# Optimization experiments

Measured on AMD Instinct MI355X. Metric: run time of the kernel, lower is better.

Reference implementation:

```python
import jax, jax.numpy as jnp
import numpy as np

OFFSET_BINS = np.array([0.0, 0.00794435329, 0.0158887021, 0.0238330509, 0.0317773996,
                        0.0397217484, 0.0476660972, 0.0556104459, 0.0635547947,
                        0.0714991435, 0.08], dtype=np.float32)
BIN_WEIGHTS = jnp.array([0.16652107, 0.21488856, 0.37031708, 0.55618503, 0.75124664,
                         0.93943357, 1.07824539, 1.19423112, 1.55731375, 2.34173634],
                        dtype=jnp.float32)
RADIUS = 0.005
FAR = 1.0e5
EPS = 1e-7


def setup_inputs():
    key = jax.random.key(0)
    ks = jax.random.split(key, 10)
    B, N, M, C = 4, 2048, 4096, 5
    return {
        'pred_grasps': jax.random.normal(ks[0], (B, N, 4, 4), jnp.float32) * 0.1,
        'pred_scores': jax.random.uniform(ks[1], (B, N, 1), jnp.float32, 1e-4, 1.0 - 1e-4),
        'pred_points': jax.random.uniform(ks[2], (B, N, 3), jnp.float32) * 0.1,
        'grasp_width_head': jax.random.normal(ks[3], (B, 10, N), jnp.float32),
        'pos_contact_points': jax.random.uniform(ks[4], (B, M, 3), jnp.float32) * 0.1,
        'pos_contact_width': jax.random.uniform(ks[5], (B, M), jnp.float32) * 0.08,
        'pos_contact_rot': jax.random.normal(ks[6], (B, M, 3, 3), jnp.float32),
        'pos_contact_trans': jax.random.uniform(ks[7], (B, M, 3), jnp.float32) * 0.1,
        'gripper_control_points': jax.random.normal(ks[8], (1, C, 3), jnp.float32) * 0.05,
        'gripper_control_points_sym': jax.random.normal(ks[9], (1, C, 3), jnp.float32) * 0.05,
        'epoch': 0,
    }


def _gather(a, idx):
    # a: (B, M, ...), idx: (B, N) -> (B, N, ...)
    return jax.vmap(lambda x, j: x[j])(a, idx)


def _pairwise_sq(a, b):
    # a: (B,N,3), b: (B,M,3) -> (B,N,M) squared distances via norm expansion
    an = jnp.sum(a * a, -1)
    bn = jnp.sum(b * b, -1)
    cross = jnp.einsum('bnd,bmd->bnm', a, b)
    return jnp.maximum(an[:, :, None] + bn[:, None, :] - 2.0 * cross, 0.0)


def _pair_min_cp(P, G):
    # P,G: (B,N,C,3) control point sets -> (B,N) min_j sum_{c,d}(P_i - G_j)^2
    pn = jnp.sum(P * P, axis=(2, 3))
    gn = jnp.sum(G * G, axis=(2, 3))
    cross = jnp.einsum('bicd,bjcd->bij', P, G)  # (B,N,N)
    sq = pn[:, :, None] + gn[:, None, :] - 2.0 * cross
    return jnp.min(sq, axis=2)


def _forward(pred_grasps, pred_scores, pred_points, grasp_width_head,
             pos_contact_points, pos_contact_width, pos_contact_rot,
             pos_contact_trans, gripper_control_points, gripper_control_points_sym):
    B, N, _ = pred_points.shape
    # ---- labels: nearest GT contact per predicted point (nsample=1) ----
    d2 = _pairwise_sq(pred_points, pos_contact_points)          # (B,N,M)
    idx = jnp.argmin(d2, axis=2)                                 # (B,N)
    min_d2 = jnp.take_along_axis(d2, idx[:, :, None], axis=2)[..., 0]
    width_label = _gather(pos_contact_width, idx)[..., None]     # (B,N,1)
    success = (min_d2 < RADIUS ** 2).astype(jnp.float32)[..., None]  # (B,N,1)
    rot_label = _gather(pos_contact_rot, idx)                    # (B,N,3,3)
    trans_label = _gather(pos_contact_trans, idx)                # (B,N,3)

    pos_in_view = jnp.clip(jnp.sum(success, axis=1), 1.0, None)  # (B,1)

    # ---- binary score loss with balanced pos/neg sampling ----
    p = jnp.clip(pred_scores, EPS, 1.0 - EPS)
    bce = -(success * jnp.log(p) + (1.0 - success) * jnp.log(1.0 - p))[..., 0]  # (B,N)
    pos = success[..., 0]
    neg = 1.0 - pos
    n_pos = jnp.sum(pos, axis=1)                                 # (B,)
    r = jax.random.uniform(jax.random.key(42), (B, N))
    pri = jnp.where(neg > 0.5, r, jnp.inf)
    rank = jnp.argsort(jnp.argsort(pri, axis=1), axis=1)         # random ranks over negatives
    k = jnp.where(n_pos > 0, n_pos, 2.0)
    sel_neg = ((rank < k[:, None]) & (neg > 0.5)).astype(jnp.float32)
    sel = pos + sel_neg
    bin_ce_loss = jnp.mean(jnp.sum(bce * sel, axis=1) / jnp.maximum(jnp.sum(sel, axis=1), 1.0))

    # ---- width loss: multihot bins + weighted BCE-with-logits ----
    lo = jnp.asarray(OFFSET_BINS[:-1])
    hi = jnp.asarray(OFFSET_BINS[1:])
    multihot = ((width_label >= lo) & (width_label < hi)).astype(jnp.float32)  # (B,N,10)
    x = jnp.transpose(grasp_width_head, (0, 2, 1))               # (B,N,10)
    bcew = jnp.maximum(x, 0.0) - x * multihot + jnp.log1p(jnp.exp(-jnp.abs(x)))
    wl = jnp.mean(BIN_WEIGHTS[None, None, :] * bcew, axis=2)     # (B,N)
    width_loss = jnp.mean(jnp.sum(wl * pos, axis=1, keepdims=True) / pos_in_view)

    # ---- ADD-S loss ----
    mask = success > 0.5                                          # (B,N,1)
    rot_l = jnp.where(mask[..., None], rot_label, FAR)
    trans_l = jnp.where(mask, trans_label, FAR)
    cp = gripper_control_points[0]                                # (C,3)
    cps = gripper_control_points_sym[0]
    pred_rot = pred_grasps[:, :, :3, :3]
    pred_trans = pred_grasps[:, :, :3, 3]
    P = jnp.einsum('bnij,cj->bnci', pred_rot, cp) + pred_trans[:, :, None, :]
    G = jnp.einsum('bnij,cj->bnci', rot_l, cp) + trans_l[:, :, None, :]
    Gs = jnp.einsum('bnij,cj->bnci', rot_l, cps) + trans_l[:, :, None, :]
    m = jnp.minimum(_pair_min_cp(P, G), _pair_min_cp(P, Gs))     # (B,N)
    min_adds = pos * jnp.sqrt(jnp.maximum(m, 0.0) + 1e-12)
    adds = jnp.sum(pred_scores[..., 0] * min_adds, axis=1) / pos_in_view[:, 0]
    adds_loss = jnp.mean(adds)

    total_loss = bin_ce_loss + width_loss + 3.0 * adds_loss
    return total_loss, bin_ce_loss, width_loss, adds_loss


def reference(pred_grasps, pred_scores, pred_points, grasp_width_head,
              pos_contact_points, pos_contact_width, pos_contact_rot,
              pos_contact_trans, gripper_control_points, gripper_control_points_sym, epoch):
    return _forward(pred_grasps, pred_scores, pred_points, grasp_width_head,
                    pos_contact_points, pos_contact_width, pos_contact_rot,
                    pos_contact_trans, gripper_control_points, gripper_control_points_sym)
```

## Files before the change

kernel.cpp:

```cpp
#include <hip/hip_runtime.h>
#include <math.h>

#define B_ 4
#define N_ 2048
#define M_ 4096

__constant__ float c_LO[10] = {0.0f, 0.00794435329f, 0.0158887021f, 0.0238330509f,
                               0.0317773996f, 0.0397217484f, 0.0476660972f,
                               0.0556104459f, 0.0635547947f, 0.0714991435f};
__constant__ float c_HI[10] = {0.00794435329f, 0.0158887021f, 0.0238330509f,
                               0.0317773996f, 0.0397217484f, 0.0476660972f,
                               0.0556104459f, 0.0635547947f, 0.0714991435f, 0.08f};
__constant__ float c_BW[10] = {0.16652107f, 0.21488856f, 0.37031708f, 0.55618503f,
                               0.75124664f, 0.93943357f, 1.07824539f, 1.19423112f,
                               1.55731375f, 2.34173634f};

#define R2_ 2.5e-05f
#define FAR_ 100000.0f
#define EPS_ 1e-07f

__device__ inline unsigned rotl32(unsigned x, int d) { return (x << d) | (x >> (32 - d)); }

__device__ inline void threefry2x32_42(unsigned x0, unsigned x1, unsigned& o0, unsigned& o1) {
    const unsigned k0 = 0u, k1 = 42u;
    const unsigned k2 = k0 ^ k1 ^ 0x1BD11BDAu;
    const unsigned ks[3] = {k0, k1, k2};
    const int rot[2][4] = {{13, 15, 26, 6}, {17, 29, 16, 24}};
    unsigned v0 = x0 + k0;
    unsigned v1 = x1 + k1;
#pragma unroll
    for (int i = 0; i < 5; ++i) {
        const int* r = rot[i & 1];
#pragma unroll
        for (int j = 0; j < 4; ++j) {
            v0 += v1;
            v1 = rotl32(v1, r[j]);
            v1 ^= v0;
        }
        v0 += ks[(i + 1) % 3];
        v1 += ks[(i + 2) % 3] + (unsigned)(i + 1);
    }
    o0 = v0; o1 = v1;
}

__device__ inline float bits_to_uniform(unsigned bits) {
    float f = __uint_as_float((bits >> 9) | 0x3f800000u) - 1.0f;
    return fmaxf(0.0f, f);
}

__device__ inline float jax_uniform_r(int flat) {
    unsigned o0, o1;
    if (flat < 4096) {
        threefry2x32_42((unsigned)flat, (unsigned)(flat + 4096), o0, o1);
        return bits_to_uniform(o0);
    } else {
        threefry2x32_42((unsigned)(flat - 4096), (unsigned)flat, o0, o1);
        return bits_to_uniform(o1);
    }
}

__global__ __launch_bounds__(256, 4) void nn_prep_kernel(
        const float* __restrict__ ppts, const float* __restrict__ pcp,
        const float* __restrict__ pred_grasps,
        const float* __restrict__ rot, const float* __restrict__ trans,
        const float* __restrict__ cp, const float* __restrict__ cps,
        int* __restrict__ idx_out, float* __restrict__ d2_out,
        float* __restrict__ Pout, float* __restrict__ Gt,
        int* __restrict__ counters) {
    if (blockIdx.x == 0 && threadIdx.x == 0) { counters[0] = 0; counters[1] = 0; }
    int blk = blockIdx.x;
    int b = blk / (N_ / 8);
    int tile = blk % (N_ / 8);
    int tid = threadIdx.x;
    int ig = tid & 1;
    int part = tid >> 1;
    int i0 = tile * 8 + ig * 4;

    float ax[4], ay[4], az[4], an[4];
#pragma unroll
    for (int ii = 0; ii < 4; ++ii) {
        const float* pp = ppts + ((size_t)b * N_ + i0 + ii) * 3;
        ax[ii] = pp[0]; ay[ii] = pp[1]; az[ii] = pp[2];
        an[ii] = ax[ii] * ax[ii] + ay[ii] * ay[ii] + az[ii] * az[ii];
    }

    const float4* pb4 = reinterpret_cast<const float4*>(pcp + (size_t)b * M_ * 3);
    float best[4] = {INFINITY, INFINITY, INFINITY, INFINITY};
    int bidx[4] = {0, 0, 0, 0};
    for (int g = 0; g < 8; ++g) {
        int grp = g * 128 + part;
        float4 q0 = pb4[grp * 3 + 0];
        float4 q1 = pb4[grp * 3 + 1];
        float4 q2 = pb4[grp * 3 + 2];
        float px[4] = {q0.x, q0.w, q1.z, q2.y};
        float py[4] = {q0.y, q1.x, q1.w, q2.z};
        float pz[4] = {q0.z, q1.y, q2.x, q2.w};
#pragma unroll
        for (int k = 0; k < 4; ++k) {
            float bn = px[k] * px[k] + py[k] * py[k] + pz[k] * pz[k];
            int j = grp * 4 + k;
#pragma unroll
            for (int ii = 0; ii < 4; ++ii) {
                float cross = ax[ii] * px[k] + ay[ii] * py[k] + az[ii] * pz[k];
                float d = an[ii] + bn - 2.0f * cross;
                d = fmaxf(d, 0.0f);
                if (d < best[ii]) { best[ii] = d; bidx[ii] = j; }
            }
        }
    }

    __shared__ float sd[8][128];
    __shared__ int si[8][128];
#pragma unroll
    for (int ii = 0; ii < 4; ++ii) {
        sd[ig * 4 + ii][part] = best[ii];
        si[ig * 4 + ii][part] = bidx[ii];
    }
    __syncthreads();

    if (tid < 8) {
        int n = tile * 8 + tid;
        float bb = INFINITY;
        int bi = 0x7fffffff;
        for (int p = 0; p < 128; ++p) {
            float dv = sd[tid][p];
            int iv = si[tid][p];
            if (dv < bb || (dv == bb && iv < bi)) { bb = dv; bi = iv; }
        }
        idx_out[b * N_ + n] = bi;
        d2_out[b * N_ + n] = bb;

        size_t i = (size_t)b * N_ + n;
        const float* g = pred_grasps + i * 16;
        float R[3][3] = {{g[0], g[1], g[2]}, {g[4], g[5], g[6]}, {g[8], g[9], g[10]}};
        float t[3] = {g[3], g[7], g[11]};

        float* P = Pout + i * 16;
        float pn = 0.0f;
#pragma unroll
        for (int c = 0; c < 5; ++c) {
            float cx = cp[c * 3], cy = cp[c * 3 + 1], cz = cp[c * 3 + 2];
#pragma unroll
            for (int kk = 0; kk < 3; ++kk) {
                float v = R[kk][0] * cx + R[kk][1] * cy + R[kk][2] * cz + t[kk];
                P[c * 3 + kk] = v;
                pn += v * v;
            }
        }
        P[15] = pn;

        bool succ = bb < R2_;
        float RL[3][3], TL[3];
        if (succ) {
            const float* rl = rot + ((size_t)b * M_ + bi) * 9;
#pragma unroll
            for (int a = 0; a < 3; ++a)
#pragma unroll
                for (int c2 = 0; c2 < 3; ++c2) RL[a][c2] = rl[a * 3 + c2];
            const float* tl = trans + ((size_t)b * M_ + bi) * 3;
            TL[0] = tl[0]; TL[1] = tl[1]; TL[2] = tl[2];
        } else {
#pragma unroll
            for (int a = 0; a < 3; ++a) {
#pragma unroll
                for (int c2 = 0; c2 < 3; ++c2) RL[a][c2] = FAR_;
                TL[a] = FAR_;
            }
        }

        float* gtb = Gt + ((size_t)b * 8 * N_ + n) * 4;
        float gn = 0.0f, gsn = 0.0f;
#pragma unroll
        for (int c = 0; c < 5; ++c) {
            float cx = cp[c * 3], cy = cp[c * 3 + 1], cz = cp[c * 3 + 2];
#pragma unroll
            for (int kk = 0; kk < 3; ++kk) {
                int comp = c * 3 + kk;
                float v = RL[kk][0] * cx + RL[kk][1] * cy + RL[kk][2] * cz + TL[kk];
                gtb[(size_t)(comp >> 2) * (N_ * 4) + (comp & 3)] = v;
                gn += v * v;
            }
        }
        gtb[(size_t)(15 >> 2) * (N_ * 4) + (15 & 3)] = gn;
#pragma unroll
        for (int c = 0; c < 5; ++c) {
            float cx = cps[c * 3], cy = cps[c * 3 + 1], cz = cps[c * 3 + 2];
#pragma unroll
            for (int kk = 0; kk < 3; ++kk) {
                int comp = 16 + c * 3 + kk;
                float v = RL[kk][0] * cx + RL[kk][1] * cy + RL[kk][2] * cz + TL[kk];
                gtb[(size_t)(comp >> 2) * (N_ * 4) + (comp & 3)] = v;
                gsn += v * v;
            }
        }
        gtb[(size_t)(31 >> 2) * (N_ * 4) + (31 & 3)] = gsn;
    }
}

__global__ __launch_bounds__(256) void rank_kernel(const float* __restrict__ d2w,
                                                   float* __restrict__ selws) {
    int blk = blockIdx.x;
    int b = blk / (N_ / 16);
    int tile = blk % (N_ / 16);
    int tid = threadIdx.x;
    int n_local = tid & 15;
    int part = tid >> 4;

    __shared__ __align__(16) float pri[N_];
    __shared__ int cnt_sh[16][17];
    __shared__ int s_npos;
    if (tid == 0) s_npos = 0;
    __syncthreads();

    int lp = 0;
    for (int q = tid; q < N_; q += 256) {
        bool pos = d2w[b * N_ + q] < R2_;
        pri[q] = pos ? INFINITY : jax_uniform_r(b * N_ + q);
        if (pos) lp++;
    }
    atomicAdd(&s_npos, lp);
    __syncthreads();

    int n = tile * 16 + n_local;
    float ra = pri[n];

    int cnt = 0;
    const float4* p4 = reinterpret_cast<const float4*>(pri);
    for (int o = 0; o < 8; ++o) {
        float4 v[4];
#pragma unroll
        for (int k = 0; k < 4; ++k) v[k] = p4[part + (o * 4 + k) * 16];
#pragma unroll
        for (int k = 0; k < 4; ++k) {
            int qb = (part + (o * 4 + k) * 16) * 4;
            cnt += ((v[k].x < ra) || (v[k].x == ra && (qb + 0) < n)) ? 1 : 0;
            cnt += ((v[k].y < ra) || (v[k].y == ra && (qb + 1) < n)) ? 1 : 0;
            cnt += ((v[k].z < ra) || (v[k].z == ra && (qb + 2) < n)) ? 1 : 0;
            cnt += ((v[k].w < ra) || (v[k].w == ra && (qb + 3) < n)) ? 1 : 0;
        }
    }
    cnt_sh[part][n_local] = cnt;
    __syncthreads();

    if (tid < 16) {
        int tot = 0;
#pragma unroll
        for (int p = 0; p < 16; ++p) tot += cnt_sh[p][tid];
        int npos = s_npos;
        int kk = (npos > 0) ? npos : 2;
        int n2 = tile * 16 + tid;
        float r2 = pri[n2];
        selws[b * N_ + n2] = (r2 == INFINITY) ? 1.0f : ((tot < kk) ? 1.0f : 0.0f);
    }
}

__global__ __launch_bounds__(256, 4) void adds_kernel(const float* __restrict__ Parr,
                                                      const float4* __restrict__ Gt4,
                                                      float* __restrict__ mOut) {
    int blk = blockIdx.x;
    int b = blk / (N_ / 8);
    int tile = blk % (N_ / 8);
    int w = threadIdx.x >> 6;
    int lane = threadIdx.x & 63;
    int i0 = tile * 8 + w * 2;

    const float4* P4 = reinterpret_cast<const float4*>(Parr) + ((size_t)b * N_ + i0) * 4;
    float Pv[2][16];
#pragma unroll
    for (int h = 0; h < 2; ++h)
#pragma unroll
        for (int q = 0; q < 4; ++q) {
            float4 v = P4[h * 4 + q];
            Pv[h][q * 4 + 0] = v.x; Pv[h][q * 4 + 1] = v.y;
            Pv[h][q * 4 + 2] = v.z; Pv[h][q * 4 + 3] = v.w;
        }

    const float4* gq = Gt4 + (size_t)b * 8 * N_;
    float best0 = INFINITY, best1 = INFINITY;
    for (int jb = 0; jb < N_ / 64; ++jb) {
        int j = jb * 64 + lane;
        float g[16];
        {
            float4 h0 = gq[(size_t)0 * N_ + j];
            float4 h1 = gq[(size_t)1 * N_ + j];
            float4 h2 = gq[(size_t)2 * N_ + j];
            float4 h3 = gq[(size_t)3 * N_ + j];
            g[0] = h0.x; g[1] = h0.y; g[2] = h0.z; g[3] = h0.w;
            g[4] = h1.x; g[5] = h1.y; g[6] = h1.z; g[7] = h1.w;
            g[8] = h2.x; g[9] = h2.y; g[10] = h2.z; g[11] = h2.w;
            g[12] = h3.x; g[13] = h3.y; g[14] = h3.z; g[15] = h3.w;
        }
        float d00 = 0.0f, d10 = 0.0f;
#pragma unroll
        for (int q = 0; q < 15; ++q) {
            d00 += Pv[0][q] * g[q];
            d10 += Pv[1][q] * g[q];
        }
        float s00 = Pv[0][15] + g[15] - 2.0f * d00;
        float s10 = Pv[1][15] + g[15] - 2.0f * d10;
        {
            float4 h0 = gq[(size_t)4 * N_ + j];
            float4 h1 = gq[(size_t)5 * N_ + j];
            float4 h2 = gq[(size_t)6 * N_ + j];
            float4 h3 = gq[(size_t)7 * N_ + j];
            g[0] = h0.x; g[1] = h0.y; g[2] = h0.z; g[3] = h0.w;
            g[4] = h1.x; g[5] = h1.y; g[6] = h1.z; g[7] = h1.w;
            g[8] = h2.x; g[9] = h2.y; g[10] = h2.z; g[11] = h2.w;
            g[12] = h3.x; g[13] = h3.y; g[14] = h3.z; g[15] = h3.w;
        }
        float d01 = 0.0f, d11 = 0.0f;
#pragma unroll
        for (int q = 0; q < 15; ++q) {
            d01 += Pv[0][q] * g[q];
            d11 += Pv[1][q] * g[q];
        }
        float s01 = Pv[0][15] + g[15] - 2.0f * d01;
        float s11 = Pv[1][15] + g[15] - 2.0f * d11;
        best0 = fminf(best0, fminf(s00, s01));
        best1 = fminf(best1, fminf(s10, s11));
    }
#pragma unroll
    for (int m = 32; m > 0; m >>= 1) {
        best0 = fminf(best0, __shfl_xor(best0, m));
        best1 = fminf(best1, __shfl_xor(best1, m));
    }
    if (lane == 0) {
        mOut[b * N_ + i0 + 0] = best0;
        mOut[b * N_ + i0 + 1] = best1;
    }
}

__global__ __launch_bounds__(256) void finalize_kernel(
        const float* __restrict__ scores, const float* __restrict__ gwh,
        const float* __restrict__ pcw, const int* __restrict__ idxw,
        const float* __restrict__ d2w, const float* __restrict__ mw,
        const float* __restrict__ selws,
        float* __restrict__ partials, int* __restrict__ counters,
        float* __restrict__ out) {
    int fid = blockIdx.x;
    int b = fid >> 3;
    int part = fid & 7;
    int tid = threadIdx.x;
    int n = part * 256 + tid;
    __shared__ float wsum[4][5];

    float sc = scores[b * N_ + n];
    float pcl = fminf(fmaxf(sc, EPS_), 0.9999999f);
    bool pos = d2w[b * N_ + n] < R2_;
    float s = pos ? 1.0f : 0.0f;
    float bce = -(s * logf(pcl) + (1.0f - s) * logf(1.0f - pcl));
    float selv = selws[b * N_ + n];
    float sum_sel = selv;
    float sum_bce = bce * selv;
    float sum_pos = s;
    float sum_wl = 0.0f, sum_adds = 0.0f;
    if (pos) {
        int jx = idxw[b * N_ + n];
        float w = pcw[b * M_ + jx];
        float acc = 0.0f;
#pragma unroll
        for (int jb = 0; jb < 10; ++jb) {
            float x = gwh[((size_t)b * 10 + jb) * N_ + n];
            float mh = (w >= c_LO[jb] && w < c_HI[jb]) ? 1.0f : 0.0f;
            float bw = fmaxf(x, 0.0f) - x * mh + log1pf(expf(-fabsf(x)));
            acc += c_BW[jb] * bw;
        }
        sum_wl = acc * 0.1f;
        float mv = mw[b * N_ + n];
        sum_adds = sc * sqrtf(fmaxf(mv, 0.0f) + 1e-12f);
    }

    float v0 = sum_sel, v1 = sum_bce, v2 = sum_wl, v3 = sum_adds, v4 = sum_pos;
#pragma unroll
    for (int off = 32; off > 0; off >>= 1) {
        v0 += __shfl_down(v0, off);
        v1 += __shfl_down(v1, off);
        v2 += __shfl_down(v2, off);
        v3 += __shfl_down(v3, off);
        v4 += __shfl_down(v4, off);
    }
    int wv = tid >> 6, lane = tid & 63;
    if (lane == 0) {
        wsum[wv][0] = v0; wsum[wv][1] = v1; wsum[wv][2] = v2;
        wsum[wv][3] = v3; wsum[wv][4] = v4;
    }
    __syncthreads();
    if (tid == 0) {
        float t0 = 0, t1 = 0, t2 = 0, t3 = 0, t4 = 0;
#pragma unroll
        for (int w = 0; w < 4; ++w) {
            t0 += wsum[w][0]; t1 += wsum[w][1]; t2 += wsum[w][2];
            t3 += wsum[w][3]; t4 += wsum[w][4];
        }
        float* pp = partials + (size_t)fid * 5;
        pp[0] = t0; pp[1] = t1; pp[2] = t2; pp[3] = t3; pp[4] = t4;
        __threadfence();
        int old = atomicAdd(&counters[1], 1);
        if (old == 32 - 1) {
            __threadfence();
            float bin = 0, wid = 0, ad = 0;
#pragma unroll
            for (int b2 = 0; b2 < B_; ++b2) {
                float u0 = 0, u1 = 0, u2 = 0, u3 = 0, u4 = 0;
#pragma unroll
                for (int p2 = 0; p2 < 8; ++p2) {
                    const float* q = partials + (size_t)(b2 * 8 + p2) * 5;
                    u0 += q[0]; u1 += q[1]; u2 += q[2]; u3 += q[3]; u4 += q[4];
                }
                float piv = fmaxf(u4, 1.0f);
                bin += u1 / fmaxf(u0, 1.0f);
                wid += u2 / piv;
                ad  += u3 / piv;
            }
            bin *= 0.25f; wid *= 0.25f; ad *= 0.25f;
            out[0] = bin + wid + 3.0f * ad;
            out[1] = bin;
            out[2] = wid;
            out[3] = ad;
        }
    }
}

extern "C" void kernel_launch(void* const* d_in, const int* in_sizes, int n_in,
                              void* d_out, int out_size, void* d_ws, size_t ws_size,
                              hipStream_t stream) {
    const float* pred_grasps = (const float*)d_in[0];
    const float* pred_scores = (const float*)d_in[1];
    const float* pred_points = (const float*)d_in[2];
    const float* gwh         = (const float*)d_in[3];
    const float* pcp         = (const float*)d_in[4];
    const float* pcw         = (const float*)d_in[5];
    const float* pcr         = (const float*)d_in[6];
    const float* pct         = (const float*)d_in[7];
    const float* cp          = (const float*)d_in[8];
    const float* cps         = (const float*)d_in[9];
    (void)in_sizes; (void)n_in; (void)out_size; (void)ws_size;

    float* ws = (float*)d_ws;
    int*   idxw  = (int*)ws;
    float* d2w   = ws + 8192;
    float* Pw    = ws + 16384;
    float* Gt    = Pw + 131072;
    float* mw    = Gt + 262144;
    float* selws = mw + 8192;
    float* parts = selws + 8192;
    int*   ctrs  = (int*)(parts + 160);
    float* outp  = (float*)d_out;

    hipLaunchKernelGGL(nn_prep_kernel, dim3(B_ * (N_ / 8)), dim3(256), 0, stream,
                       pred_points, pcp, pred_grasps, pcr, pct, cp, cps,
                       idxw, d2w, Pw, Gt, ctrs);
    hipLaunchKernelGGL(rank_kernel, dim3(B_ * (N_ / 16)), dim3(256), 0, stream,
                       d2w, selws);
    hipLaunchKernelGGL(adds_kernel, dim3(B_ * (N_ / 8)), dim3(256), 0, stream,
                       Pw, (const float4*)Gt, mw);
    hipLaunchKernelGGL(finalize_kernel, dim3(B_ * 8), dim3(256), 0, stream,
                       pred_scores, gwh, pcw, idxw, d2w, mw, selws, parts, ctrs, outp);
}
```

Baseline: 152.4 us.

## Prepack contact points with norms and merge rank and ADDS kernels into one launch

Adds a small pre-pass that packs the contact points into float4 (x,y,z,|p|^2), so the nearest-neighbour loop reads one aligned vector per point and no longer recomputes norms. The independent rank and ADDS kernels are merged into one grid, with block index choosing the role, so they run concurrently and one launch is saved. This adds an extra launch and workspace traffic for the packing pass. The merged kernel also carries the union of both roles' register and shared-memory needs, which may lower occupancy for the ADDS blocks.

```diff
diff --git a/kernel.cpp b/kernel.cpp
--- a/kernel.cpp
+++ b/kernel.cpp
@@ -4,6 +4,9 @@
 #define B_ 4
 #define N_ 2048
 #define M_ 4096
+
+#define ADDS_BLOCKS (B_ * (N_ / 8))
+#define RANK_BLOCKS (B_ * (N_ / 16))
 
 __constant__ float c_LO[10] = {0.0f, 0.00794435329f, 0.0158887021f, 0.0238330509f,
                                0.0317773996f, 0.0397217484f, 0.0476660972f,
@@ -59,15 +62,25 @@
     }
 }
 
+__global__ __launch_bounds__(256) void pack_contacts(const float* __restrict__ pts,
+                                                     float4* __restrict__ out,
+                                                     int* __restrict__ counters) {
+    int i = blockIdx.x * blockDim.x + threadIdx.x;
+    if (i == 0) { counters[0] = 0; counters[1] = 0; }
+    if (i >= B_ * M_) return;
+    float x = pts[(size_t)i * 3 + 0];
+    float y = pts[(size_t)i * 3 + 1];
+    float z = pts[(size_t)i * 3 + 2];
+    out[i] = make_float4(x, y, z, x * x + y * y + z * z);
+}
+
 __global__ __launch_bounds__(256, 4) void nn_prep_kernel(
-        const float* __restrict__ ppts, const float* __restrict__ pcp,
+        const float* __restrict__ ppts, const float4* __restrict__ cpack,
         const float* __restrict__ pred_grasps,
         const float* __restrict__ rot, const float* __restrict__ trans,
         const float* __restrict__ cp, const float* __restrict__ cps,
         int* __restrict__ idx_out, float* __restrict__ d2_out,
-        float* __restrict__ Pout, float* __restrict__ Gt,
-        int* __restrict__ counters) {
-    if (blockIdx.x == 0 && threadIdx.x == 0) { counters[0] = 0; counters[1] = 0; }
+        float* __restrict__ Pout, float* __restrict__ Gt) {
     int blk = blockIdx.x;
     int b = blk / (N_ / 8);
     int tile = blk % (N_ / 8);
@@ -84,25 +97,20 @@
         an[ii] = ax[ii] * ax[ii] + ay[ii] * ay[ii] + az[ii] * az[ii];
     }
 
-    const float4* pb4 = reinterpret_cast<const float4*>(pcp + (size_t)b * M_ * 3);
+    const float4* cb = cpack + (size_t)b * M_;
     float best[4] = {INFINITY, INFINITY, INFINITY, INFINITY};
     int bidx[4] = {0, 0, 0, 0};
-    for (int g = 0; g < 8; ++g) {
-        int grp = g * 128 + part;
-        float4 q0 = pb4[grp * 3 + 0];
-        float4 q1 = pb4[grp * 3 + 1];
-        float4 q2 = pb4[grp * 3 + 2];
-        float px[4] = {q0.x, q0.w, q1.z, q2.y};
-        float py[4] = {q0.y, q1.x, q1.w, q2.z};
-        float pz[4] = {q0.z, q1.y, q2.x, q2.w};
+    for (int jj = 0; jj < 32; jj += 4) {
+        float4 q4[4];
+#pragma unroll
+        for (int k = 0; k < 4; ++k) q4[k] = cb[(jj + k) * 128 + part];
 #pragma unroll
         for (int k = 0; k < 4; ++k) {
-            float bn = px[k] * px[k] + py[k] * py[k] + pz[k] * pz[k];
-            int j = grp * 4 + k;
+            int j = (jj + k) * 128 + part;
 #pragma unroll
             for (int ii = 0; ii < 4; ++ii) {
-                float cross = ax[ii] * px[k] + ay[ii] * py[k] + az[ii] * pz[k];
-                float d = an[ii] + bn - 2.0f * cross;
+                float cross = ax[ii] * q4[k].x + ay[ii] * q4[k].y + az[ii] * q4[k].z;
+                float d = an[ii] + q4[k].w - 2.0f * cross;
                 d = fmaxf(d, 0.0f);
                 if (d < best[ii]) { best[ii] = d; bidx[ii] = j; }
             }
@@ -197,136 +205,139 @@
     }
 }
 
-__global__ __launch_bounds__(256) void rank_kernel(const float* __restrict__ d2w,
-                                                   float* __restrict__ selws) {
-    int blk = blockIdx.x;
-    int b = blk / (N_ / 16);
-    int tile = blk % (N_ / 16);
+__global__ __launch_bounds__(256, 4) void work_kernel(
+        const float* __restrict__ Parr, const float4* __restrict__ Gt4,
+        float* __restrict__ mOut,
+        const float* __restrict__ d2w, float* __restrict__ selws) {
+    __shared__ __align__(16) char smem[9600];
+    int bid = blockIdx.x;
     int tid = threadIdx.x;
-    int n_local = tid & 15;
-    int part = tid >> 4;
-
-    __shared__ __align__(16) float pri[N_];
-    __shared__ int cnt_sh[16][17];
-    __shared__ int s_npos;
-    if (tid == 0) s_npos = 0;
-    __syncthreads();
-
-    int lp = 0;
-    for (int q = tid; q < N_; q += 256) {
-        bool pos = d2w[b * N_ + q] < R2_;
-        pri[q] = pos ? INFINITY : jax_uniform_r(b * N_ + q);
-        if (pos) lp++;
-    }
-    atomicAdd(&s_npos, lp);
-    __syncthreads();
-
-    int n = tile * 16 + n_local;
-    float ra = pri[n];
-
-    int cnt = 0;
-    const float4* p4 = reinterpret_cast<const float4*>(pri);
-    for (int o = 0; o < 8; ++o) {
-        float4 v[4];
-#pragma unroll
-        for (int k = 0; k < 4; ++k) v[k] = p4[part + (o * 4 + k) * 16];
-#pragma unroll
-        for (int k = 0; k < 4; ++k) {
-            int qb = (part + (o * 4 + k) * 16) * 4;
-            cnt += ((v[k].x < ra) || (v[k].x == ra && (qb + 0) < n)) ? 1 : 0;
-            cnt += ((v[k].y < ra) || (v[k].y == ra && (qb + 1) < n)) ? 1 : 0;
-            cnt += ((v[k].z < ra) || (v[k].z == ra && (qb + 2) < n)) ? 1 : 0;
-            cnt += ((v[k].w < ra) || (v[k].w == ra && (qb + 3) < n)) ? 1 : 0;
-        }
-    }
-    cnt_sh[part][n_local] = cnt;
-    __syncthreads();
-
-    if (tid < 16) {
-        int tot = 0;
-#pragma unroll
-        for (int p = 0; p < 16; ++p) tot += cnt_sh[p][tid];
-        int npos = s_npos;
-        int kk = (npos > 0) ? npos : 2;
-        int n2 = tile * 16 + tid;
-        float r2 = pri[n2];
-        selws[b * N_ + n2] = (r2 == INFINITY) ? 1.0f : ((tot < kk) ? 1.0f : 0.0f);
-    }
-}
-
-__global__ __launch_bounds__(256, 4) void adds_kernel(const float* __restrict__ Parr,
-                                                      const float4* __restrict__ Gt4,
-                                                      float* __restrict__ mOut) {
-    int blk = blockIdx.x;
-    int b = blk / (N_ / 8);
-    int tile = blk % (N_ / 8);
-    int w = threadIdx.x >> 6;
-    int lane = threadIdx.x & 63;
-    int i0 = tile * 8 + w * 2;
-
-    const float4* P4 = reinterpret_cast<const float4*>(Parr) + ((size_t)b * N_ + i0) * 4;
-    float Pv[2][16];
-#pragma unroll
-    for (int h = 0; h < 2; ++h)
-#pragma unroll
-        for (int q = 0; q < 4; ++q) {
-            float4 v = P4[h * 4 + q];
-            Pv[h][q * 4 + 0] = v.x; Pv[h][q * 4 + 1] = v.y;
-            Pv[h][q * 4 + 2] = v.z; Pv[h][q * 4 + 3] = v.w;
-        }
-
-    const float4* gq = Gt4 + (size_t)b * 8 * N_;
-    float best0 = INFINITY, best1 = INFINITY;
-    for (int jb = 0; jb < N_ / 64; ++jb) {
-        int j = jb * 64 + lane;
-        float g[16];
-        {
-            float4 h0 = gq[(size_t)0 * N_ + j];
-            float4 h1 = gq[(size_t)1 * N_ + j];
-            float4 h2 = gq[(size_t)2 * N_ + j];
-            float4 h3 = gq[(size_t)3 * N_ + j];
-            g[0] = h0.x; g[1] = h0.y; g[2] = h0.z; g[3] = h0.w;
-            g[4] = h1.x; g[5] = h1.y; g[6] = h1.z; g[7] = h1.w;
-            g[8] = h2.x; g[9] = h2.y; g[10] = h2.z; g[11] = h2.w;
-            g[12] = h3.x; g[13] = h3.y; g[14] = h3.z; g[15] = h3.w;
-        }
-        float d00 = 0.0f, d10 = 0.0f;
-#pragma unroll
-        for (int q = 0; q < 15; ++q) {
-            d00 += Pv[0][q] * g[q];
-            d10 += Pv[1][q] * g[q];
-        }
-        float s00 = Pv[0][15] + g[15] - 2.0f * d00;
-        float s10 = Pv[1][15] + g[15] - 2.0f * d10;
-        {
-            float4 h0 = gq[(size_t)4 * N_ + j];
-            float4 h1 = gq[(size_t)5 * N_ + j];
-            float4 h2 = gq[(size_t)6 * N_ + j];
-            float4 h3 = gq[(size_t)7 * N_ + j];
-            g[0] = h0.x; g[1] = h0.y; g[2] = h0.z; g[3] = h0.w;
-            g[4] = h1.x; g[5] = h1.y; g[6] = h1.z; g[7] = h1.w;
-            g[8] = h2.x; g[9] = h2.y; g[10] = h2.z; g[11] = h2.w;
-            g[12] = h3.x; g[13] = h3.y; g[14] = h3.z; g[15] = h3.w;
-        }
-        float d01 = 0.0f, d11 = 0.0f;
-#pragma unroll
-        for (int q = 0; q < 15; ++q) {
-            d01 += Pv[0][q] * g[q];
-            d11 += Pv[1][q] * g[q];
-        }
-        float s01 = Pv[0][15] + g[15] - 2.0f * d01;
-        float s11 = Pv[1][15] + g[15] - 2.0f * d11;
-        best0 = fminf(best0, fminf(s00, s01));
-        best1 = fminf(best1, fminf(s10, s11));
-    }
-#pragma unroll
-    for (int m = 32; m > 0; m >>= 1) {
-        best0 = fminf(best0, __shfl_xor(best0, m));
-        best1 = fminf(best1, __shfl_xor(best1, m));
-    }
-    if (lane == 0) {
-        mOut[b * N_ + i0 + 0] = best0;
-        mOut[b * N_ + i0 + 1] = best1;
+
+    if (bid < ADDS_BLOCKS) {
+        int b = bid >> 8;
+        int tile = bid & 255;
+        int w = tid >> 6;
+        int lane = tid & 63;
+        int i0 = tile * 8 + w * 2;
+
+        const float4* P4 = reinterpret_cast<const float4*>(Parr) +
+                           ((size_t)b * N_ + i0) * 4;
+        float Pv[2][16];
+#pragma unroll
+        for (int h = 0; h < 2; ++h)
+#pragma unroll
+            for (int q = 0; q < 4; ++q) {
+                float4 v = P4[h * 4 + q];
+                Pv[h][q * 4 + 0] = v.x; Pv[h][q * 4 + 1] = v.y;
+                Pv[h][q * 4 + 2] = v.z; Pv[h][q * 4 + 3] = v.w;
+            }
+
+        const float4* gq = Gt4 + (size_t)b * 8 * N_;
+        float best0 = INFINITY, best1 = INFINITY;
+        for (int jb = 0; jb < N_ / 64; ++jb) {
+            int j = jb * 64 + lane;
+            float g[16];
+            {
+                float4 h0 = gq[(size_t)0 * N_ + j];
+                float4 h1 = gq[(size_t)1 * N_ + j];
+                float4 h2 = gq[(size_t)2 * N_ + j];
+                float4 h3 = gq[(size_t)3 * N_ + j];
+                g[0] = h0.x; g[1] = h0.y; g[2] = h0.z; g[3] = h0.w;
+                g[4] = h1.x; g[5] = h1.y; g[6] = h1.z; g[7] = h1.w;
+                g[8] = h2.x; g[9] = h2.y; g[10] = h2.z; g[11] = h2.w;
+                g[12] = h3.x; g[13] = h3.y; g[14] = h3.z; g[15] = h3.w;
+            }
+            float d00 = 0.0f, d10 = 0.0f;
+#pragma unroll
+            for (int q = 0; q < 15; ++q) {
+                d00 += Pv[0][q] * g[q];
+                d10 += Pv[1][q] * g[q];
+            }
+            float s00 = Pv[0][15] + g[15] - 2.0f * d00;
+            float s10 = Pv[1][15] + g[15] - 2.0f * d10;
+            {
+                float4 h0 = gq[(size_t)4 * N_ + j];
+                float4 h1 = gq[(size_t)5 * N_ + j];
+                float4 h2 = gq[(size_t)6 * N_ + j];
+                float4 h3 = gq[(size_t)7 * N_ + j];
+                g[0] = h0.x; g[1] = h0.y; g[2] = h0.z; g[3] = h0.w;
+                g[4] = h1.x; g[5] = h1.y; g[6] = h1.z; g[7] = h1.w;
+                g[8] = h2.x; g[9] = h2.y; g[10] = h2.z; g[11] = h2.w;
+                g[12] = h3.x; g[13] = h3.y; g[14] = h3.z; g[15] = h3.w;
+            }
+            float d01 = 0.0f, d11 = 0.0f;
+#pragma unroll
+            for (int q = 0; q < 15; ++q) {
+                d01 += Pv[0][q] * g[q];
+                d11 += Pv[1][q] * g[q];
+            }
+            float s01 = Pv[0][15] + g[15] - 2.0f * d01;
+            float s11 = Pv[1][15] + g[15] - 2.0f * d11;
+            best0 = fminf(best0, fminf(s00, s01));
+            best1 = fminf(best1, fminf(s10, s11));
+        }
+#pragma unroll
+        for (int m = 32; m > 0; m >>= 1) {
+            best0 = fminf(best0, __shfl_xor(best0, m));
+            best1 = fminf(best1, __shfl_xor(best1, m));
+        }
+        if (lane == 0) {
+            mOut[b * N_ + i0 + 0] = best0;
+            mOut[b * N_ + i0 + 1] = best1;
+        }
+    } else {
+        int rid = bid - ADDS_BLOCKS;
+        int b = rid / (N_ / 16);
+        int tile = rid % (N_ / 16);
+        int n_local = tid & 15;
+        int part = tid >> 4;
+
+        float* pri = (float*)smem;
+        int* cnt_sh = (int*)(smem + 8192);
+        __shared__ int s_npos;
+        if (tid == 0) s_npos = 0;
+        __syncthreads();
+
+        int lp = 0;
+        for (int q = tid; q < N_; q += 256) {
+            bool pos = d2w[b * N_ + q] < R2_;
+            pri[q] = pos ? INFINITY : jax_uniform_r(b * N_ + q);
+            if (pos) lp++;
+        }
+        atomicAdd(&s_npos, lp);
+        __syncthreads();
+
+        int n = tile * 16 + n_local;
+        float ra = pri[n];
+
+        int cnt = 0;
+        const float4* p4 = reinterpret_cast<const float4*>(pri);
+        for (int o = 0; o < 8; ++o) {
+            float4 v[4];
+#pragma unroll
+            for (int k = 0; k < 4; ++k) v[k] = p4[part + (o * 4 + k) * 16];
+#pragma unroll
+            for (int k = 0; k < 4; ++k) {
+                int qb = (part + (o * 4 + k) * 16) * 4;
+                cnt += ((v[k].x < ra) || (v[k].x == ra && (qb + 0) < n)) ? 1 : 0;
+                cnt += ((v[k].y < ra) || (v[k].y == ra && (qb + 1) < n)) ? 1 : 0;
+                cnt += ((v[k].z < ra) || (v[k].z == ra && (qb + 2) < n)) ? 1 : 0;
+                cnt += ((v[k].w < ra) || (v[k].w == ra && (qb + 3) < n)) ? 1 : 0;
+            }
+        }
+        cnt_sh[part * 17 + n_local] = cnt;
+        __syncthreads();
+
+        if (tid < 16) {
+            int tot = 0;
+#pragma unroll
+            for (int p = 0; p < 16; ++p) tot += cnt_sh[p * 17 + tid];
+            int npos = s_npos;
+            int kk = (npos > 0) ? npos : 2;
+            int n2 = tile * 16 + tid;
+            float r2 = pri[n2];
+            selws[b * N_ + n2] = (r2 == INFINITY) ? 1.0f : ((tot < kk) ? 1.0f : 0.0f);
+        }
     }
 }
 
@@ -437,9 +448,10 @@
     (void)in_sizes; (void)n_in; (void)out_size; (void)ws_size;
 
     float* ws = (float*)d_ws;
-    int*   idxw  = (int*)ws;
-    float* d2w   = ws + 8192;
-    float* Pw    = ws + 16384;
+    float4* cpack = (float4*)ws;
+    int*   idxw  = (int*)(ws + 65536);
+    float* d2w   = ws + 65536 + 8192;
+    float* Pw    = ws + 65536 + 16384;
     float* Gt    = Pw + 131072;
     float* mw    = Gt + 262144;
     float* selws = mw + 8192;
@@ -447,13 +459,13 @@
     int*   ctrs  = (int*)(parts + 160);
     float* outp  = (float*)d_out;
 
+    hipLaunchKernelGGL(pack_contacts, dim3((B_ * M_ + 255) / 256), dim3(256), 0, stream,
+                       pcp, cpack, ctrs);
     hipLaunchKernelGGL(nn_prep_kernel, dim3(B_ * (N_ / 8)), dim3(256), 0, stream,
-                       pred_points, pcp, pred_grasps, pcr, pct, cp, cps,
-                       idxw, d2w, Pw, Gt, ctrs);
-    hipLaunchKernelGGL(rank_kernel, dim3(B_ * (N_ / 16)), dim3(256), 0, stream,
-                       d2w, selws);
-    hipLaunchKernelGGL(adds_kernel, dim3(B_ * (N_ / 8)), dim3(256), 0, stream,
-                       Pw, (const float4*)Gt, mw);
+                       pred_points, cpack, pred_grasps, pcr, pct, cp, cps,
+                       idxw, d2w, Pw, Gt);
+    hipLaunchKernelGGL(work_kernel, dim3(ADDS_BLOCKS + RANK_BLOCKS), dim3(256), 0, stream,
+                       Pw, (const float4*)Gt, mw, d2w, selws);
     hipLaunchKernelGGL(finalize_kernel, dim3(B_ * 8), dim3(256), 0, stream,
                        pred_scores, gwh, pcw, idxw, d2w, mw, selws, parts, ctrs, outp);
 }
```

Result: slower. 176.2 us (+15.6%).
